# Kernel optimization log

Hardware: AMD Instinct MI355X
Metric: run time of the kernel (lower is better)

The kernel has to match this reference:

```python
import jax, jax.numpy as jnp
import numpy as np

RESID = 1024
HEADS = 16
HEAD_DIM = 64


def setup_inputs() -> dict:
    key = jax.random.key(0)
    ks = jax.random.split(key, 6)
    B, S = 2, 2048
    residual_stream = jax.random.normal(ks[0], (B, S, RESID), dtype=jnp.float32)
    # per-head qkv linear params, stacked over heads: [H, resid, 3*head_dim]
    W_qkv = jax.random.normal(ks[1], (HEADS, RESID, 3 * HEAD_DIM), dtype=jnp.float32) * (1.0 / np.sqrt(RESID))
    b_qkv = jax.random.normal(ks[2], (HEADS, 3 * HEAD_DIM), dtype=jnp.float32) * 0.01
    # output projection resid -> resid
    W_o = jax.random.normal(ks[3], (RESID, RESID), dtype=jnp.float32) * (1.0 / np.sqrt(RESID))
    b_o = jax.random.normal(ks[4], (RESID,), dtype=jnp.float32) * 0.01
    return {"residual_stream": residual_stream, "W_qkv": W_qkv, "b_qkv": b_qkv, "W_o": W_o, "b_o": b_o}


def reference(residual_stream, W_qkv, b_qkv, W_o, b_o):
    # qkv per head: [B, H, S, 3*D]
    qkv = jnp.einsum('bsr,hrd->bhsd', residual_stream, W_qkv) + b_qkv[None, :, None, :]
    q = qkv[..., :HEAD_DIM]
    k = qkv[..., HEAD_DIM:2 * HEAD_DIM]
    v = qkv[..., 2 * HEAD_DIM:]
    # NOTE: original has no causal mask; softmax over full key axis
    scores = jnp.einsum('bhsd,bhtd->bhst', q, k) / jnp.sqrt(jnp.float32(HEAD_DIM))
    attn = jax.nn.softmax(scores, axis=-1)
    out = jnp.einsum('bhst,bhtd->bhsd', attn, v)  # [B, H, S, D]
    B, H, S, D = out.shape
    out = out.transpose(0, 2, 1, 3).reshape(B, S, H * D)  # concat heads -> [B, S, resid]
    return out @ W_o + b_o
```

## Files before the change

### kernel.cpp

```cpp
#include <hip/hip_runtime.h>
#include <hip/hip_bf16.h>

#define B_ 2
#define S_ 2048
#define H_ 16
#define HD 64
#define R_ 1024
#define N_ (B_*S_)

typedef unsigned short ushort_t;
typedef short bf16x8 __attribute__((ext_vector_type(8)));
typedef float f32x4 __attribute__((ext_vector_type(4)));

#define MFMA(a,b,c) __builtin_amdgcn_mfma_f32_16x16x32_bf16(a,b,c,0,0,0)
#define GLD16(g,l) __builtin_amdgcn_global_load_lds( \
    (const __attribute__((address_space(1))) void*)(g), \
    (__attribute__((address_space(3))) void*)(l), 16, 0, 0)

__device__ __forceinline__ unsigned short f2bf(float f) {
  unsigned int u = __builtin_bit_cast(unsigned int, f);
  u += 0x7fffu + ((u >> 16) & 1u);
  return (unsigned short)(u >> 16);
}

__device__ __forceinline__ bf16x8 ld8(const ushort_t* p) {
  return *(const bf16x8*)p;
}

__global__ __launch_bounds__(256) void k_convert_x(const float* __restrict__ x,
                                                   ushort_t* __restrict__ xb) {
  int i = blockIdx.x * 256 + threadIdx.x;
  float4 v = ((const float4*)x)[i];
  ushort4 o;
  o.x = f2bf(v.x); o.y = f2bf(v.y); o.z = f2bf(v.z); o.w = f2bf(v.w);
  ((ushort4*)xb)[i] = o;
}

__global__ __launch_bounds__(256) void k_transpose(const float* __restrict__ in,
                                                   ushort_t* __restrict__ out,
                                                   int rows, int cols) {
  __shared__ float t[64][65];
  const size_t bo = (size_t)blockIdx.z * rows * cols;
  const int r0 = blockIdx.x * 64, c0 = blockIdx.y * 64;
  const int tx = threadIdx.x & 63, ty = threadIdx.x >> 6;
  #pragma unroll
  for (int i = 0; i < 16; i++) {
    int r = ty * 16 + i;
    t[r][tx] = in[bo + (size_t)(r0 + r) * cols + c0 + tx];
  }
  __syncthreads();
  #pragma unroll
  for (int i = 0; i < 16; i++) {
    int c = ty * 16 + i;
    out[bo + (size_t)(c0 + c) * rows + r0 + tx] = f2bf(t[tx][c]);
  }
}

__global__ __launch_bounds__(256, 2) void k_qkv(
    const ushort_t* __restrict__ Xb, const ushort_t* __restrict__ WT,
    const float* __restrict__ bqkv,
    ushort_t* __restrict__ Q, ushort_t* __restrict__ K, ushort_t* __restrict__ Vt) {
  __shared__ ushort_t lA[2][128 * 32];
  __shared__ ushort_t lB[2][192 * 32];
  const int m0 = blockIdx.x * 128;
  const int h  = blockIdx.y;
  const int tid = threadIdx.x;
  const int w = tid >> 6, l = tid & 63;
  const int lr = l & 15, lg = l >> 4;
  const int wr = w >> 1, wc = w & 1;

  const ushort_t* Asrc = Xb + (size_t)m0 * R_;
  const ushort_t* Bsrc = WT + (size_t)h * 192 * R_;
  const int arow = l >> 2;
  const int acol = (l & 3) * 8;

  f32x4 acc[4][6];
  const f32x4 fz = {0.f, 0.f, 0.f, 0.f};
  #pragma unroll
  for (int m = 0; m < 4; m++)
    #pragma unroll
    for (int n = 0; n < 6; n++) acc[m][n] = fz;

  auto stage = [&](int buf, int kt) {
    const int k0 = kt * 32;
    #pragma unroll
    for (int i = 0; i < 2; i++) {
      int chunk = w + 4 * i;
      GLD16(Asrc + (size_t)(chunk * 16 + arow) * R_ + k0 + acol, &lA[buf][chunk * 512]);
    }
    #pragma unroll
    for (int i = 0; i < 3; i++) {
      int chunk = w + 4 * i;
      GLD16(Bsrc + (size_t)(chunk * 16 + arow) * R_ + k0 + acol, &lB[buf][chunk * 512]);
    }
  };

  stage(0, 0);
  asm volatile("s_waitcnt vmcnt(0)" ::: "memory");
  __syncthreads();

  int cur = 0;
  for (int kt = 0; kt < 32; ++kt) {
    if (kt < 31) stage(cur ^ 1, kt + 1);
    bf16x8 af[4], bfr[6];
    #pragma unroll
    for (int m = 0; m < 4; m++)
      af[m] = ld8(&lA[cur][(wr * 64 + m * 16 + lr) * 32 + lg * 8]);
    #pragma unroll
    for (int n = 0; n < 6; n++)
      bfr[n] = ld8(&lB[cur][(wc * 96 + n * 16 + lr) * 32 + lg * 8]);
    __builtin_amdgcn_s_setprio(1);
    #pragma unroll
    for (int m = 0; m < 4; m++)
      #pragma unroll
      for (int n = 0; n < 6; n++)
        acc[m][n] = MFMA(af[m], bfr[n], acc[m][n]);
    __builtin_amdgcn_s_setprio(0);
    asm volatile("s_waitcnt vmcnt(0)" ::: "memory");
    __syncthreads();
    cur ^= 1;
  }

  #pragma unroll
  for (int n = 0; n < 6; n++) {
    const int col = wc * 96 + n * 16 + lr;
    const float bias = bqkv[h * 192 + col];
    #pragma unroll
    for (int m = 0; m < 4; m++) {
      const int rb = m0 + wr * 64 + m * 16 + lg * 4;
      #pragma unroll
      for (int r = 0; r < 4; r++) {
        float v = acc[m][n][r] + bias;
        int srow = rb + r;
        int b = srow >> 11, s = srow & 2047;
        size_t bh = (size_t)b * H_ + h;
        if (col < 64) {
          Q[(bh * S_ + s) * HD + col] = f2bf(v * 0.125f);
        } else if (col < 128) {
          int d = col - 64;
          K[(bh * S_ + s) * HD + (d ^ ((s & 7) << 3))] = f2bf(v);
        } else {
          int d = col - 128;
          Vt[(bh * HD + d) * S_ + (s ^ ((d & 7) << 3))] = f2bf(v);
        }
      }
    }
  }
}

__global__ __launch_bounds__(256, 2) void k_attn(
    const ushort_t* __restrict__ Q, const ushort_t* __restrict__ K,
    const ushort_t* __restrict__ Vt, ushort_t* __restrict__ AO) {
  __shared__ ushort_t lK[2][64 * 64];
  __shared__ ushort_t lV[2][64 * 64];
  __shared__ ushort_t lP[4][32 * 72];
  const int qt = blockIdx.x;
  const int bh = blockIdx.y;
  const int b = bh >> 4, h = bh & 15;
  const int tid = threadIdx.x, w = tid >> 6, l = tid & 63;
  const int lr = l & 15, lg = l >> 4;

  const ushort_t* Qb = Q + (size_t)bh * S_ * HD;
  const ushort_t* Kb = K + (size_t)bh * S_ * HD;
  const ushort_t* Vb = Vt + (size_t)bh * HD * S_;

  bf16x8 qf[2][2];
  #pragma unroll
  for (int m = 0; m < 2; m++) {
    int row = qt * 128 + 32 * w + m * 16 + lr;
    qf[m][0] = ld8(&Qb[(size_t)row * HD + lg * 8]);
    qf[m][1] = ld8(&Qb[(size_t)row * HD + 32 + lg * 8]);
  }

  auto stage = [&](int buf, int t0) {
    #pragma unroll
    for (int i = 0; i < 2; i++) {
      int chunk = w + 4 * i;
      int r = chunk * 8 + (l >> 3);
      int c = (l & 7) * 8;
      GLD16(&Kb[(size_t)(t0 + r) * HD + c], &lK[buf][chunk * 512]);
      GLD16(&Vb[(size_t)r * S_ + t0 + c], &lV[buf][chunk * 512]);
    }
  };

  const f32x4 fz = {0.f, 0.f, 0.f, 0.f};
  const bf16x8 onesv = {0x3F80, 0x3F80, 0x3F80, 0x3F80, 0x3F80, 0x3F80, 0x3F80, 0x3F80};
  f32x4 oacc[2][4];
  f32x4 ss[2];
  #pragma unroll
  for (int m = 0; m < 2; m++) {
    ss[m] = fz;
    #pragma unroll
    for (int n = 0; n < 4; n++) oacc[m][n] = fz;
  }

  stage(0, 0);
  asm volatile("s_waitcnt vmcnt(0)" ::: "memory");
  __syncthreads();

  int cur = 0;
  for (int kt = 0; kt < 32; ++kt) {
    if (kt < 31) stage(cur ^ 1, (kt + 1) * 64);

    bf16x8 kb[4][2];
    #pragma unroll
    for (int n = 0; n < 4; n++) {
      kb[n][0] = ld8(&lK[cur][(n * 16 + lr) * 64 + ((0 + lg) ^ (lr & 7)) * 8]);
      kb[n][1] = ld8(&lK[cur][(n * 16 + lr) * 64 + ((4 + lg) ^ (lr & 7)) * 8]);
    }

    f32x4 sc[2][4];
    __builtin_amdgcn_s_setprio(1);
    #pragma unroll
    for (int m = 0; m < 2; m++)
      #pragma unroll
      for (int n = 0; n < 4; n++) {
        f32x4 t = fz;
        t = MFMA(qf[m][0], kb[n][0], t);
        t = MFMA(qf[m][1], kb[n][1], t);
        sc[m][n] = t;
      }
    __builtin_amdgcn_s_setprio(0);

    #pragma unroll
    for (int m = 0; m < 2; m++)
      #pragma unroll
      for (int n = 0; n < 4; n++)
        #pragma unroll
        for (int r = 0; r < 4; r++) {
          float p = __expf(sc[m][n][r]);
          lP[w][(m * 16 + lg * 4 + r) * 72 + n * 16 + lr] = f2bf(p);
        }

    bf16x8 pa[2][2];
    #pragma unroll
    for (int m = 0; m < 2; m++) {
      pa[m][0] = ld8(&lP[w][(m * 16 + lr) * 72 + lg * 8]);
      pa[m][1] = ld8(&lP[w][(m * 16 + lr) * 72 + 32 + lg * 8]);
    }

    __builtin_amdgcn_s_setprio(1);
    #pragma unroll
    for (int n = 0; n < 4; n++) {
      bf16x8 vb0 = ld8(&lV[cur][(n * 16 + lr) * 64 + ((0 + lg) ^ (lr & 7)) * 8]);
      bf16x8 vb1 = ld8(&lV[cur][(n * 16 + lr) * 64 + ((4 + lg) ^ (lr & 7)) * 8]);
      #pragma unroll
      for (int m = 0; m < 2; m++) {
        oacc[m][n] = MFMA(pa[m][0], vb0, oacc[m][n]);
        oacc[m][n] = MFMA(pa[m][1], vb1, oacc[m][n]);
      }
    }
    #pragma unroll
    for (int m = 0; m < 2; m++) {
      ss[m] = MFMA(pa[m][0], onesv, ss[m]);
      ss[m] = MFMA(pa[m][1], onesv, ss[m]);
    }
    __builtin_amdgcn_s_setprio(0);

    asm volatile("s_waitcnt vmcnt(0)" ::: "memory");
    __syncthreads();
    cur ^= 1;
  }

  #pragma unroll
  for (int m = 0; m < 2; m++)
    #pragma unroll
    for (int r = 0; r < 4; r++) {
      int s = qt * 128 + 32 * w + m * 16 + lg * 4 + r;
      float inv = 1.0f / ss[m][r];
      #pragma unroll
      for (int n = 0; n < 4; n++) {
        float o = oacc[m][n][r] * inv;
        AO[(size_t)(b * S_ + s) * R_ + h * HD + n * 16 + lr] = f2bf(o);
      }
    }
}

__global__ __launch_bounds__(256, 2) void k_out(
    const ushort_t* __restrict__ AO, const ushort_t* __restrict__ WoT,
    const float* __restrict__ bo, float* __restrict__ out) {
  __shared__ ushort_t lA[2][128 * 32];
  __shared__ ushort_t lB[2][128 * 32];
  const int m0 = blockIdx.x * 128, n0 = blockIdx.y * 128;
  const int tid = threadIdx.x, w = tid >> 6, l = tid & 63;
  const int lr = l & 15, lg = l >> 4;
  const int wr = w >> 1, wc = w & 1;
  const ushort_t* Asrc = AO + (size_t)m0 * R_;
  const ushort_t* Bsrc = WoT + (size_t)n0 * R_;
  const int arow = l >> 2, acol = (l & 3) * 8;

  f32x4 acc[4][4];
  const f32x4 fz = {0.f, 0.f, 0.f, 0.f};
  #pragma unroll
  for (int m = 0; m < 4; m++)
    #pragma unroll
    for (int n = 0; n < 4; n++) acc[m][n] = fz;

  auto stage = [&](int buf, int kt) {
    const int k0 = kt * 32;
    #pragma unroll
    for (int i = 0; i < 2; i++) {
      int chunk = w + 4 * i;
      GLD16(Asrc + (size_t)(chunk * 16 + arow) * R_ + k0 + acol, &lA[buf][chunk * 512]);
      GLD16(Bsrc + (size_t)(chunk * 16 + arow) * R_ + k0 + acol, &lB[buf][chunk * 512]);
    }
  };

  stage(0, 0);
  asm volatile("s_waitcnt vmcnt(0)" ::: "memory");
  __syncthreads();

  int cur = 0;
  for (int kt = 0; kt < 32; ++kt) {
    if (kt < 31) stage(cur ^ 1, kt + 1);
    bf16x8 af[4], bfr[4];
    #pragma unroll
    for (int m = 0; m < 4; m++)
      af[m] = ld8(&lA[cur][(wr * 64 + m * 16 + lr) * 32 + lg * 8]);
    #pragma unroll
    for (int n = 0; n < 4; n++)
      bfr[n] = ld8(&lB[cur][(wc * 64 + n * 16 + lr) * 32 + lg * 8]);
    __builtin_amdgcn_s_setprio(1);
    #pragma unroll
    for (int m = 0; m < 4; m++)
      #pragma unroll
      for (int n = 0; n < 4; n++)
        acc[m][n] = MFMA(af[m], bfr[n], acc[m][n]);
    __builtin_amdgcn_s_setprio(0);
    asm volatile("s_waitcnt vmcnt(0)" ::: "memory");
    __syncthreads();
    cur ^= 1;
  }

  #pragma unroll
  for (int n = 0; n < 4; n++) {
    const int col = n0 + wc * 64 + n * 16 + lr;
    const float bias = bo[col];
    #pragma unroll
    for (int m = 0; m < 4; m++) {
      const int row = m0 + wr * 64 + m * 16 + lg * 4;
      #pragma unroll
      for (int r = 0; r < 4; r++)
        out[(size_t)(row + r) * R_ + col] = acc[m][n][r] + bias;
    }
  }
}

extern "C" void kernel_launch(void* const* d_in, const int* in_sizes, int n_in,
                              void* d_out, int out_size, void* d_ws, size_t ws_size,
                              hipStream_t stream) {
  const float* resid = (const float*)d_in[0];
  const float* Wqkv  = (const float*)d_in[1];
  const float* bqkv  = (const float*)d_in[2];
  const float* Wo    = (const float*)d_in[3];
  const float* bo    = (const float*)d_in[4];
  float* out = (float*)d_out;

  ushort_t* Xb  = (ushort_t*)d_ws;
  ushort_t* WT  = Xb  + (size_t)N_ * R_;
  ushort_t* WoT = WT  + (size_t)H_ * 192 * R_;
  ushort_t* Qd  = WoT + (size_t)R_ * R_;
  ushort_t* Kd  = Qd  + (size_t)B_ * H_ * S_ * HD;
  ushort_t* Vtd = Kd  + (size_t)B_ * H_ * S_ * HD;
  ushort_t* AOd = Vtd + (size_t)B_ * H_ * S_ * HD;

  k_convert_x<<<dim3(4096), dim3(256), 0, stream>>>(resid, Xb);
  k_transpose<<<dim3(16, 3, 16), dim3(256), 0, stream>>>(Wqkv, WT, 1024, 192);
  k_transpose<<<dim3(16, 16, 1), dim3(256), 0, stream>>>(Wo, WoT, 1024, 1024);
  k_qkv<<<dim3(32, 16), dim3(256), 0, stream>>>(Xb, WT, bqkv, Qd, Kd, Vtd);
  k_attn<<<dim3(16, 32), dim3(256), 0, stream>>>(Qd, Kd, Vtd, AOd);
  k_out<<<dim3(32, 8), dim3(256), 0, stream>>>(AOd, WoT, bo, out);
}
```

Measured before the change: 135.5 us.

## Use 32x32 MFMA in attention and keep P in registers via lane shuffles

Rewrites the attention inner loop around 32x32x16 bf16 MFMAs, computing S^T so that exp'd probabilities can be packed with v_cvt_pk_bf16 and exchanged across half-waves with shuffles instead of round-tripping through LDS. Q is prescaled by log2(e)/sqrt(D) so exp2f replaces __expf. This removes the per-wave P staging buffer and its LDS stores and loads. In exchange it adds cross-lane shuffles and a more complex output index mapping, and it keeps the existing lack of max subtraction.

```diff
diff --git a/kernel.cpp b/kernel.cpp
--- a/kernel.cpp
+++ b/kernel.cpp
@@ -11,8 +11,10 @@
 typedef unsigned short ushort_t;
 typedef short bf16x8 __attribute__((ext_vector_type(8)));
 typedef float f32x4 __attribute__((ext_vector_type(4)));
+typedef float f32x16 __attribute__((ext_vector_type(16)));
 
 #define MFMA(a,b,c) __builtin_amdgcn_mfma_f32_16x16x32_bf16(a,b,c,0,0,0)
+#define MFMA32(a,b,c) __builtin_amdgcn_mfma_f32_32x32x16_bf16(a,b,c,0,0,0)
 #define GLD16(g,l) __builtin_amdgcn_global_load_lds( \
     (const __attribute__((address_space(1))) void*)(g), \
     (__attribute__((address_space(3))) void*)(l), 16, 0, 0)
@@ -21,6 +23,12 @@
   unsigned int u = __builtin_bit_cast(unsigned int, f);
   u += 0x7fffu + ((u >> 16) & 1u);
   return (unsigned short)(u >> 16);
+}
+
+__device__ __forceinline__ unsigned int cvtpk(float lo, float hi) {
+  unsigned int r;
+  asm("v_cvt_pk_bf16_f32 %0, %1, %2" : "=v"(r) : "v"(lo), "v"(hi));
+  return r;
 }
 
 __device__ __forceinline__ bf16x8 ld8(const ushort_t* p) {
@@ -135,7 +143,7 @@
         int b = srow >> 11, s = srow & 2047;
         size_t bh = (size_t)b * H_ + h;
         if (col < 64) {
-          Q[(bh * S_ + s) * HD + col] = f2bf(v * 0.125f);
+          Q[(bh * S_ + s) * HD + col] = f2bf(v * 0.1803368801111137f);
         } else if (col < 128) {
           int d = col - 64;
           K[(bh * S_ + s) * HD + (d ^ ((s & 7) << 3))] = f2bf(v);
@@ -153,23 +161,22 @@
     const ushort_t* __restrict__ Vt, ushort_t* __restrict__ AO) {
   __shared__ ushort_t lK[2][64 * 64];
   __shared__ ushort_t lV[2][64 * 64];
-  __shared__ ushort_t lP[4][32 * 72];
   const int qt = blockIdx.x;
   const int bh = blockIdx.y;
   const int b = bh >> 4, h = bh & 15;
   const int tid = threadIdx.x, w = tid >> 6, l = tid & 63;
-  const int lr = l & 15, lg = l >> 4;
+  const int lq = l & 31, hi = l >> 5;
 
   const ushort_t* Qb = Q + (size_t)bh * S_ * HD;
   const ushort_t* Kb = K + (size_t)bh * S_ * HD;
   const ushort_t* Vb = Vt + (size_t)bh * HD * S_;
 
-  bf16x8 qf[2][2];
-  #pragma unroll
-  for (int m = 0; m < 2; m++) {
-    int row = qt * 128 + 32 * w + m * 16 + lr;
-    qf[m][0] = ld8(&Qb[(size_t)row * HD + lg * 8]);
-    qf[m][1] = ld8(&Qb[(size_t)row * HD + 32 + lg * 8]);
+  bf16x8 qf[4];
+  {
+    int qrow = qt * 128 + 32 * w + lq;
+    #pragma unroll
+    for (int kd = 0; kd < 4; kd++)
+      qf[kd] = ld8(&Qb[(size_t)qrow * HD + kd * 16 + hi * 8]);
   }
 
   auto stage = [&](int buf, int t0) {
@@ -183,16 +190,13 @@
     }
   };
 
-  const f32x4 fz = {0.f, 0.f, 0.f, 0.f};
+  const f32x16 fz16 = {0};
   const bf16x8 onesv = {0x3F80, 0x3F80, 0x3F80, 0x3F80, 0x3F80, 0x3F80, 0x3F80, 0x3F80};
-  f32x4 oacc[2][4];
-  f32x4 ss[2];
-  #pragma unroll
-  for (int m = 0; m < 2; m++) {
-    ss[m] = fz;
-    #pragma unroll
-    for (int n = 0; n < 4; n++) oacc[m][n] = fz;
-  }
+  f32x16 oacc[2];
+  f32x16 ss;
+  oacc[0] = fz16; oacc[1] = fz16; ss = fz16;
+
+  const int swz = (lq & 7) * 8;
 
   stage(0, 0);
   asm volatile("s_waitcnt vmcnt(0)" ::: "memory");
@@ -202,58 +206,54 @@
   for (int kt = 0; kt < 32; ++kt) {
     if (kt < 31) stage(cur ^ 1, (kt + 1) * 64);
 
-    bf16x8 kb[4][2];
-    #pragma unroll
-    for (int n = 0; n < 4; n++) {
-      kb[n][0] = ld8(&lK[cur][(n * 16 + lr) * 64 + ((0 + lg) ^ (lr & 7)) * 8]);
-      kb[n][1] = ld8(&lK[cur][(n * 16 + lr) * 64 + ((4 + lg) ^ (lr & 7)) * 8]);
-    }
-
-    f32x4 sc[2][4];
+    f32x16 sc[2];
+    sc[0] = fz16; sc[1] = fz16;
     __builtin_amdgcn_s_setprio(1);
     #pragma unroll
-    for (int m = 0; m < 2; m++)
-      #pragma unroll
-      for (int n = 0; n < 4; n++) {
-        f32x4 t = fz;
-        t = MFMA(qf[m][0], kb[n][0], t);
-        t = MFMA(qf[m][1], kb[n][1], t);
-        sc[m][n] = t;
+    for (int kd = 0; kd < 4; kd++) {
+      bf16x8 ka0 = ld8(&lK[cur][(lq) * 64 + ((kd * 16 + hi * 8) ^ swz)]);
+      bf16x8 ka1 = ld8(&lK[cur][(32 + lq) * 64 + ((kd * 16 + hi * 8) ^ swz)]);
+      sc[0] = MFMA32(ka0, qf[kd], sc[0]);
+      sc[1] = MFMA32(ka1, qf[kd], sc[1]);
+    }
+    __builtin_amdgcn_s_setprio(0);
+
+    unsigned int pk[2][4], pq[2][4], px[2][4], pxq[2][4];
+    #pragma unroll
+    for (int n = 0; n < 2; n++)
+      #pragma unroll
+      for (int b2 = 0; b2 < 4; b2++) {
+        float e0 = exp2f(sc[n][4 * b2 + 0]);
+        float e1 = exp2f(sc[n][4 * b2 + 1]);
+        float e2 = exp2f(sc[n][4 * b2 + 2]);
+        float e3 = exp2f(sc[n][4 * b2 + 3]);
+        pk[n][b2] = cvtpk(e0, e1);
+        pq[n][b2] = cvtpk(e2, e3);
       }
-    __builtin_amdgcn_s_setprio(0);
-
-    #pragma unroll
-    for (int m = 0; m < 2; m++)
-      #pragma unroll
-      for (int n = 0; n < 4; n++)
-        #pragma unroll
-        for (int r = 0; r < 4; r++) {
-          float p = __expf(sc[m][n][r]);
-          lP[w][(m * 16 + lg * 4 + r) * 72 + n * 16 + lr] = f2bf(p);
-        }
-
-    bf16x8 pa[2][2];
-    #pragma unroll
-    for (int m = 0; m < 2; m++) {
-      pa[m][0] = ld8(&lP[w][(m * 16 + lr) * 72 + lg * 8]);
-      pa[m][1] = ld8(&lP[w][(m * 16 + lr) * 72 + 32 + lg * 8]);
-    }
+    #pragma unroll
+    for (int n = 0; n < 2; n++)
+      #pragma unroll
+      for (int b2 = 0; b2 < 4; b2++) {
+        px[n][b2]  = __shfl_xor((int)pk[n][b2], 32, 64);
+        pxq[n][b2] = __shfl_xor((int)pq[n][b2], 32, 64);
+      }
 
     __builtin_amdgcn_s_setprio(1);
     #pragma unroll
-    for (int n = 0; n < 4; n++) {
-      bf16x8 vb0 = ld8(&lV[cur][(n * 16 + lr) * 64 + ((0 + lg) ^ (lr & 7)) * 8]);
-      bf16x8 vb1 = ld8(&lV[cur][(n * 16 + lr) * 64 + ((4 + lg) ^ (lr & 7)) * 8]);
-      #pragma unroll
-      for (int m = 0; m < 2; m++) {
-        oacc[m][n] = MFMA(pa[m][0], vb0, oacc[m][n]);
-        oacc[m][n] = MFMA(pa[m][1], vb1, oacc[m][n]);
+    for (int ks = 0; ks < 4; ks++) {
+      const int n = ks >> 1, k1 = (ks & 1) * 2;
+      unsigned int w0 = hi ? px[n][k1 + 1]  : pk[n][k1];
+      unsigned int w1 = hi ? pxq[n][k1 + 1] : pq[n][k1];
+      unsigned int w2 = hi ? pk[n][k1 + 1]  : px[n][k1];
+      unsigned int w3 = hi ? pq[n][k1 + 1]  : pxq[n][k1];
+      int4 wv = {(int)w0, (int)w1, (int)w2, (int)w3};
+      bf16x8 pa = __builtin_bit_cast(bf16x8, wv);
+      ss = MFMA32(pa, onesv, ss);
+      #pragma unroll
+      for (int db = 0; db < 2; db++) {
+        bf16x8 vb = ld8(&lV[cur][(db * 32 + lq) * 64 + ((ks * 16 + hi * 8) ^ swz)]);
+        oacc[db] = MFMA32(pa, vb, oacc[db]);
       }
-    }
-    #pragma unroll
-    for (int m = 0; m < 2; m++) {
-      ss[m] = MFMA(pa[m][0], onesv, ss[m]);
-      ss[m] = MFMA(pa[m][1], onesv, ss[m]);
     }
     __builtin_amdgcn_s_setprio(0);
 
@@ -262,17 +262,17 @@
     cur ^= 1;
   }
 
-  #pragma unroll
-  for (int m = 0; m < 2; m++)
-    #pragma unroll
-    for (int r = 0; r < 4; r++) {
-      int s = qt * 128 + 32 * w + m * 16 + lg * 4 + r;
-      float inv = 1.0f / ss[m][r];
-      #pragma unroll
-      for (int n = 0; n < 4; n++) {
-        float o = oacc[m][n][r] * inv;
-        AO[(size_t)(b * S_ + s) * R_ + h * HD + n * 16 + lr] = f2bf(o);
-      }
+  float inv[16];
+  #pragma unroll
+  for (int reg = 0; reg < 16; reg++) inv[reg] = 1.0f / ss[reg];
+  #pragma unroll
+  for (int db = 0; db < 2; db++)
+    #pragma unroll
+    for (int reg = 0; reg < 16; reg++) {
+      int qloc = (reg & 3) + 8 * (reg >> 2) + 4 * hi;
+      int s = qt * 128 + 32 * w + qloc;
+      float o = oacc[db][reg] * inv[reg];
+      AO[(size_t)(b * S_ + s) * R_ + h * HD + db * 32 + lq] = f2bf(o);
     }
 }
 
```

Result: slower. 140.0 us (+3.3%).

## Load K/V tiles directly into registers and drop LDS staging in attention

Applied to the files above, without the earlier changes.

The attention kernel stops staging K and V tiles through shared memory with global_load_lds and barriers. Each wave now loads its K and V MFMA operands straight from global memory into registers, double-buffered across iterations, and the swizzled K/Vt layouts are removed from the QKV kernel. The softmax exponent becomes exp2 by folding log2(e) into the Q scale. This removes LDS traffic and per-tile __syncthreads, but every wave now reads the full K/V tile from global/L2 on its own, which raises global traffic about fourfold and register pressure.

```diff
diff --git a/kernel.cpp b/kernel.cpp
--- a/kernel.cpp
+++ b/kernel.cpp
@@ -135,13 +135,13 @@
         int b = srow >> 11, s = srow & 2047;
         size_t bh = (size_t)b * H_ + h;
         if (col < 64) {
-          Q[(bh * S_ + s) * HD + col] = f2bf(v * 0.125f);
+          Q[(bh * S_ + s) * HD + col] = f2bf(v * 0.1803368801111137f);
         } else if (col < 128) {
           int d = col - 64;
-          K[(bh * S_ + s) * HD + (d ^ ((s & 7) << 3))] = f2bf(v);
+          K[(bh * S_ + s) * HD + d] = f2bf(v);
         } else {
           int d = col - 128;
-          Vt[(bh * HD + d) * S_ + (s ^ ((d & 7) << 3))] = f2bf(v);
+          Vt[(bh * HD + d) * S_ + s] = f2bf(v);
         }
       }
     }
@@ -151,8 +151,6 @@
 __global__ __launch_bounds__(256, 2) void k_attn(
     const ushort_t* __restrict__ Q, const ushort_t* __restrict__ K,
     const ushort_t* __restrict__ Vt, ushort_t* __restrict__ AO) {
-  __shared__ ushort_t lK[2][64 * 64];
-  __shared__ ushort_t lV[2][64 * 64];
   __shared__ ushort_t lP[4][32 * 72];
   const int qt = blockIdx.x;
   const int bh = blockIdx.y;
@@ -172,17 +170,6 @@
     qf[m][1] = ld8(&Qb[(size_t)row * HD + 32 + lg * 8]);
   }
 
-  auto stage = [&](int buf, int t0) {
-    #pragma unroll
-    for (int i = 0; i < 2; i++) {
-      int chunk = w + 4 * i;
-      int r = chunk * 8 + (l >> 3);
-      int c = (l & 7) * 8;
-      GLD16(&Kb[(size_t)(t0 + r) * HD + c], &lK[buf][chunk * 512]);
-      GLD16(&Vb[(size_t)r * S_ + t0 + c], &lV[buf][chunk * 512]);
-    }
-  };
-
   const f32x4 fz = {0.f, 0.f, 0.f, 0.f};
   const bf16x8 onesv = {0x3F80, 0x3F80, 0x3F80, 0x3F80, 0x3F80, 0x3F80, 0x3F80, 0x3F80};
   f32x4 oacc[2][4];
@@ -194,21 +181,17 @@
     for (int n = 0; n < 4; n++) oacc[m][n] = fz;
   }
 
-  stage(0, 0);
-  asm volatile("s_waitcnt vmcnt(0)" ::: "memory");
-  __syncthreads();
-
-  int cur = 0;
-  for (int kt = 0; kt < 32; ++kt) {
-    if (kt < 31) stage(cur ^ 1, (kt + 1) * 64);
-
-    bf16x8 kb[4][2];
-    #pragma unroll
-    for (int n = 0; n < 4; n++) {
-      kb[n][0] = ld8(&lK[cur][(n * 16 + lr) * 64 + ((0 + lg) ^ (lr & 7)) * 8]);
-      kb[n][1] = ld8(&lK[cur][(n * 16 + lr) * 64 + ((4 + lg) ^ (lr & 7)) * 8]);
-    }
-
+  auto loadKV = [&](int t0, bf16x8 kb[4][2], bf16x8 vb[4][2]) {
+    #pragma unroll
+    for (int n = 0; n < 4; n++)
+      #pragma unroll
+      for (int h32 = 0; h32 < 2; h32++) {
+        kb[n][h32] = ld8(&Kb[(size_t)(t0 + n * 16 + lr) * HD + h32 * 32 + lg * 8]);
+        vb[n][h32] = ld8(&Vb[(size_t)(n * 16 + lr) * S_ + t0 + h32 * 32 + lg * 8]);
+      }
+  };
+
+  auto compute = [&](bf16x8 kb[4][2], bf16x8 vb[4][2]) {
     f32x4 sc[2][4];
     __builtin_amdgcn_s_setprio(1);
     #pragma unroll
@@ -228,7 +211,7 @@
       for (int n = 0; n < 4; n++)
         #pragma unroll
         for (int r = 0; r < 4; r++) {
-          float p = __expf(sc[m][n][r]);
+          float p = exp2f(sc[m][n][r]);
           lP[w][(m * 16 + lg * 4 + r) * 72 + n * 16 + lr] = f2bf(p);
         }
 
@@ -241,25 +224,27 @@
 
     __builtin_amdgcn_s_setprio(1);
     #pragma unroll
-    for (int n = 0; n < 4; n++) {
-      bf16x8 vb0 = ld8(&lV[cur][(n * 16 + lr) * 64 + ((0 + lg) ^ (lr & 7)) * 8]);
-      bf16x8 vb1 = ld8(&lV[cur][(n * 16 + lr) * 64 + ((4 + lg) ^ (lr & 7)) * 8]);
+    for (int n = 0; n < 4; n++)
       #pragma unroll
       for (int m = 0; m < 2; m++) {
-        oacc[m][n] = MFMA(pa[m][0], vb0, oacc[m][n]);
-        oacc[m][n] = MFMA(pa[m][1], vb1, oacc[m][n]);
-      }
-    }
+        oacc[m][n] = MFMA(pa[m][0], vb[n][0], oacc[m][n]);
+        oacc[m][n] = MFMA(pa[m][1], vb[n][1], oacc[m][n]);
+      }
     #pragma unroll
     for (int m = 0; m < 2; m++) {
       ss[m] = MFMA(pa[m][0], onesv, ss[m]);
       ss[m] = MFMA(pa[m][1], onesv, ss[m]);
     }
     __builtin_amdgcn_s_setprio(0);
-
-    asm volatile("s_waitcnt vmcnt(0)" ::: "memory");
-    __syncthreads();
-    cur ^= 1;
+  };
+
+  bf16x8 kbA[4][2], vbA[4][2], kbB[4][2], vbB[4][2];
+  loadKV(0, kbA, vbA);
+  for (int kt = 0; kt < 32; kt += 2) {
+    loadKV((kt + 1) * 64, kbB, vbB);
+    compute(kbA, vbA);
+    if (kt + 2 < 32) loadKV((kt + 2) * 64, kbA, vbA);
+    compute(kbB, vbB);
   }
 
   #pragma unroll
```

Measured after the change: 198.8 us. 46.7% more time.
